# Kernel optimization log

Measured on AMD Instinct MI355X. Metric: run time of the kernel, lower is better.

Reference implementation:

```python
import jax, jax.numpy as jnp
import numpy as np

H_DIM = 768
NUM_HEADS = 12
HEAD_DIM = H_DIM // NUM_HEADS
ROPE_BASE = 10000.0


def rope_cos_sin(seq_len, dim):
    inv_freq = 1.0 / (ROPE_BASE ** (jnp.arange(0, dim, 2, dtype=jnp.float32) / dim))
    t = jnp.arange(seq_len, dtype=jnp.float32)
    freqs = jnp.outer(t, inv_freq)              # [seq, dim/2]
    emb = jnp.concatenate([freqs, freqs], axis=-1)  # [seq, dim]
    return jnp.cos(emb), jnp.sin(emb)


def rotate_half(x):
    x1, x2 = jnp.split(x, 2, axis=-1)
    return jnp.concatenate([-x2, x1], axis=-1)


def setup_inputs() -> dict:
    key = jax.random.key(0)
    ks = jax.random.split(key, 9)
    s = 1.0 / np.sqrt(H_DIM)
    inp = {
        'x': jax.random.normal(ks[0], (2, 8, 1024, H_DIM), dtype=jnp.float32),
        'Wq': jax.random.normal(ks[1], (H_DIM, H_DIM), dtype=jnp.float32) * s,
        'bq': jnp.zeros((H_DIM,), dtype=jnp.float32),
        'Wk': jax.random.normal(ks[2], (H_DIM, H_DIM), dtype=jnp.float32) * s,
        'bk': jnp.zeros((H_DIM,), dtype=jnp.float32),
        'Wv': jax.random.normal(ks[3], (H_DIM, H_DIM), dtype=jnp.float32) * s,
        'bv': jnp.zeros((H_DIM,), dtype=jnp.float32),
        'Wo': jax.random.normal(ks[4], (H_DIM, H_DIM), dtype=jnp.float32) * s,
        'bo': jnp.zeros((H_DIM,), dtype=jnp.float32),
        'mask': jnp.ones((2, 8, 1, 1, 1024), dtype=jnp.int32),
    }
    return inp


def reference(x, Wq, bq, Wk, bk, Wv, bv, Wo, bo, mask):
    b, r, s, d = x.shape
    H, D = NUM_HEADS, HEAD_DIM

    def proj(W, bvec):
        # [b,r,s,d] -> [b,r,H,s,D]
        y = x @ W + bvec
        return y.reshape(b, r, s, H, D).transpose(0, 1, 3, 2, 4)

    q = proj(Wq, bq)
    k = proj(Wk, bk)
    v = proj(Wv, bv)

    cos, sin = rope_cos_sin(s, D)   # [s, D]
    cos = cos[None, None, None]     # broadcast over b,r,H
    sin = sin[None, None, None]
    q = q * cos + rotate_half(q) * sin
    k = k * cos + rotate_half(k) * sin

    scores = jnp.einsum('brhqd,brhkd->brhqk', q, k) / jnp.sqrt(jnp.float32(D))
    scores = jnp.where(mask == 0, -jnp.inf, scores)
    probs = jax.nn.softmax(scores, axis=-1)  # dropout is identity in eval
    out = jnp.einsum('brhqk,brhkd->brhqd', probs, v)
    out = out.transpose(0, 1, 3, 2, 4).reshape(b, r, s, d)
    return out @ Wo + bo
```

## Files before the change

### kernel.cpp

```cpp
#include <hip/hip_runtime.h>


#define M_TOT 16384
#define DM    768
#define NH    12
#define HD    64
#define SEQ   1024

typedef __attribute__((ext_vector_type(8))) __bf16 bf16x8;
typedef __attribute__((ext_vector_type(4))) __bf16 bf16x4;
typedef __attribute__((ext_vector_type(4))) short s16x4;
typedef __attribute__((ext_vector_type(4))) float  f32x4;

static __device__ __forceinline__ unsigned short f2b(float f) {
  unsigned u = __builtin_bit_cast(unsigned, f);
  u += 0x7FFFu + ((u >> 16) & 1u);
  return (unsigned short)(u >> 16);
}
static __device__ __forceinline__ float b2f(unsigned short s) {
  unsigned u = ((unsigned)s) << 16;
  return __builtin_bit_cast(float, u);
}
static __device__ __forceinline__ unsigned cvt_pk_bf16(float lo, float hi) {
  unsigned d;
  asm("v_cvt_pk_bf16_f32 %0, %1, %2" : "=v"(d) : "v"(lo), "v"(hi));
  return d;
}
#define MAX3(a, b, c) fmaxf(fmaxf((a), (b)), (c))

static __device__ __forceinline__ f32x4 mfma16(uint2 a, uint2 b, f32x4 c) {
#if __has_builtin(__builtin_amdgcn_mfma_f32_16x16x16_bf16)
  union U { uint2 u; bf16x4 v; } A, B;
  A.u = a; B.u = b;
  return __builtin_amdgcn_mfma_f32_16x16x16_bf16(A.v, B.v, c, 0, 0, 0);
#else
  union U { uint2 u; s16x4 v; } A, B;
  A.u = a; B.u = b;
  return __builtin_amdgcn_mfma_f32_16x16x16bf16_1k(A.v, B.v, c, 0, 0, 0);
#endif
}

static __device__ __forceinline__ void gl_lds16(const void* g, void* l) {
  __builtin_amdgcn_global_load_lds(
      (const __attribute__((address_space(1))) unsigned*)g,
      (__attribute__((address_space(3))) unsigned*)l, 16, 0, 0);
}

static __device__ __forceinline__ int swz_src(int c) {
  return ((c >> 3) << 6) + (((c & 7) ^ ((c >> 3) & 7)) << 3);
}
static __device__ __forceinline__ int swz_rd(int row, int col16) {
  return (row << 6) + ((col16 ^ (row & 7)) << 3);
}

__global__ void cvt_x(const float* __restrict__ x, unsigned short* __restrict__ xb) {
  const int n4 = M_TOT * DM / 4;
  for (int i = blockIdx.x * blockDim.x + threadIdx.x; i < n4; i += gridDim.x * blockDim.x) {
    float4 v = ((const float4*)x)[i];
    ushort4 o;
    o.x = f2b(v.x); o.y = f2b(v.y); o.z = f2b(v.z); o.w = f2b(v.w);
    ((ushort4*)xb)[i] = o;
  }
}

__global__ void prep_w(const float* __restrict__ Wq, const float* __restrict__ Wk,
                       const float* __restrict__ Wv, const float* __restrict__ Wo,
                       unsigned short* __restrict__ Wt) {
  __shared__ float T[64][65];
  const int wsel = blockIdx.z;
  const float* W = wsel == 0 ? Wq : wsel == 1 ? Wk : wsel == 2 ? Wv : Wo;
  const int k0 = blockIdx.x * 64, n0 = blockIdx.y * 64;
  const int t = threadIdx.x;
#pragma unroll
  for (int p = 0; p < 16; ++p) {
    int e = p * 256 + t, r = e >> 6, c = e & 63;
    T[r][c] = W[(size_t)(k0 + r) * DM + n0 + c];
  }
  __syncthreads();
  unsigned short* dst = Wt + (size_t)wsel * DM * DM;
#pragma unroll
  for (int p = 0; p < 16; ++p) {
    int e = p * 256 + t, r = e >> 6, c = e & 63;
    dst[(size_t)(n0 + r) * DM + k0 + c] = f2b(T[c][r]);
  }
}

__global__ void rope_tab(float* __restrict__ cosT, float* __restrict__ sinT) {
  int i = blockIdx.x * blockDim.x + threadIdx.x;
  int s = i >> 5, j = i & 31;
  float inv = powf(10000.0f, -(float)j * (1.0f / 32.0f));
  float ang = (float)s * inv;
  cosT[i] = cosf(ang);
  sinT[i] = sinf(ang);
}

__global__ void bias_cat(const float* __restrict__ bq, const float* __restrict__ bk,
                         const float* __restrict__ bv, float* __restrict__ bcat) {
  int i = blockIdx.x * 256 + threadIdx.x;
  if (i < 3 * DM)
    bcat[i] = i < DM ? bq[i] : (i < 2 * DM ? bk[i - DM] : bv[i - 2 * DM]);
}

static __device__ __forceinline__ void gemm_core(const unsigned short* __restrict__ A,
                                                 const unsigned short* __restrict__ Bt,
                                                 int m0, int n0, f32x4 acc[4][4],
                                                 char* smem) {
  unsigned short* As = (unsigned short*)smem;
  unsigned short* Bs = As + 128 * 64;
  const int tid = threadIdx.x, lane = tid & 63, w = tid >> 6;
  const int wr = w >> 1, wc = w & 1;
  const int lr = lane & 15, g4 = lane >> 4;

#pragma unroll
  for (int i = 0; i < 4; ++i)
#pragma unroll
    for (int j = 0; j < 4; ++j) acc[i][j] = (f32x4){0.f, 0.f, 0.f, 0.f};

  for (int kt = 0; kt < DM / 64; ++kt) {
    const int k0 = kt * 64;
#pragma unroll
    for (int p = 0; p < 4; ++p) {
      int cb = p * 256 + w * 64;
      int c = cb + lane;
      gl_lds16(A + (size_t)(m0 + (c >> 3)) * DM + k0 + (c & 7) * 8, (char*)As + cb * 16);
      gl_lds16(Bt + (size_t)(n0 + (c >> 3)) * DM + k0 + (c & 7) * 8, (char*)Bs + cb * 16);
    }
    __syncthreads();
#pragma unroll
    for (int kk = 0; kk < 2; ++kk) {
      const int ko = kk * 32 + g4 * 8;
      bf16x8 a[4], b[4];
#pragma unroll
      for (int i = 0; i < 4; ++i) a[i] = *(const bf16x8*)&As[(wr * 64 + i * 16 + lr) * 64 + ko];
#pragma unroll
      for (int j = 0; j < 4; ++j) b[j] = *(const bf16x8*)&Bs[(wc * 64 + j * 16 + lr) * 64 + ko];
#pragma unroll
      for (int i = 0; i < 4; ++i)
#pragma unroll
        for (int j = 0; j < 4; ++j)
          acc[i][j] = __builtin_amdgcn_mfma_f32_16x16x32_bf16(a[i], b[j], acc[i][j], 0, 0, 0);
    }
    __syncthreads();
  }
}

__global__ __launch_bounds__(256, 4) void gemm_qkv(
    const unsigned short* __restrict__ xb, const unsigned short* __restrict__ Wt,
    const float* __restrict__ bcat, const float* __restrict__ cosT,
    const float* __restrict__ sinT, unsigned short* __restrict__ Qh,
    unsigned short* __restrict__ Kh, unsigned short* __restrict__ Vt) {
  __shared__ alignas(16) char smem[32768];
  const int id = blockIdx.x;
  const int xcdc = id & 7, rem = id >> 3;
  const int y = rem % 18, xc = rem / 18;
  const int xm = xc * 8 + xcdc;
  const int m0 = xm * 128, n0 = y * 128;
  f32x4 acc[4][4];
  gemm_core(xb, Wt, m0, n0, acc, smem);

  const int tid = threadIdx.x, lane = tid & 63, w = tid >> 6;
  const int wr = w >> 1, wc = w & 1;
  const int lr = lane & 15, g4 = lane >> 4;
  const int zone = y / 6;
  const int wcol0 = n0 - zone * DM + wc * 64;
  const int h = wcol0 >> 6;
  const int br = m0 >> 10;
  const int s_base = (m0 & 1023) + wr * 64;

  if (zone == 2) {
    unsigned short* dstb = Vt + ((size_t)(br * NH + h) * HD) * SEQ;
#pragma unroll
    for (int j = 0; j < 4; ++j) {
      const int d = j * 16 + lr;
      const float bv = bcat[n0 + wc * 64 + d];
#pragma unroll
      for (int i = 0; i < 4; ++i) {
        const int s0 = s_base + i * 16 + g4 * 4;
        ushort4 st;
        st.x = f2b(acc[i][j][0] + bv);
        st.y = f2b(acc[i][j][1] + bv);
        st.z = f2b(acc[i][j][2] + bv);
        st.w = f2b(acc[i][j][3] + bv);
        *(ushort4*)&dstb[(size_t)d * SEQ + s0] = st;
      }
    }
  } else {
    const float sc = zone == 0 ? 0.125f * 1.44269504f : 1.0f;
    unsigned short* dstb = (zone ? Kh : Qh) + ((size_t)(br * NH + h) * SEQ) * HD;
    char* Wb = smem + (size_t)w * 8192;
    const int s_q = s_base + lane;
    const int bcol = n0 + wc * 64;

#pragma unroll
    for (int hh = 0; hh < 2; ++hh) {
#pragma unroll
      for (int jj = 0; jj < 2; ++jj) {
        const int jp = hh + jj * 2;
        const float bv = bcat[bcol + jp * 16 + lr];
        const int dslot = jj * 16 + lr;
        const int sub = (dslot & 3) * 4;
        const int ch = dslot >> 2;
#pragma unroll
        for (int i = 0; i < 4; ++i) {
#pragma unroll
          for (int r = 0; r < 4; ++r) {
            const int s_loc = i * 16 + g4 * 4 + r;
            *(float*)(Wb + s_loc * 128 + ((ch ^ (s_loc & 7)) << 4) + sub) =
                (acc[i][jp][r] + bv) * sc;
          }
        }
      }
      unsigned short* drow = dstb + (size_t)s_q * HD + hh * 16;
      const char* Rb = Wb + lane * 128;
      const int lx = lane & 7;
#pragma unroll
      for (int c = 0; c < 4; ++c) {
        f32x4 va = *(const f32x4*)(Rb + ((c ^ lx) << 4));
        f32x4 vb = *(const f32x4*)(Rb + (((c + 4) ^ lx) << 4));
        float4 c4 = *(const float4*)&cosT[s_q * 32 + hh * 16 + c * 4];
        float4 s4 = *(const float4*)&sinT[s_q * 32 + hh * 16 + c * 4];
        uint2 oa, ob;
        oa.x = cvt_pk_bf16(va[0] * c4.x - vb[0] * s4.x, va[1] * c4.y - vb[1] * s4.y);
        oa.y = cvt_pk_bf16(va[2] * c4.z - vb[2] * s4.z, va[3] * c4.w - vb[3] * s4.w);
        ob.x = cvt_pk_bf16(vb[0] * c4.x + va[0] * s4.x, vb[1] * c4.y + va[1] * s4.y);
        ob.y = cvt_pk_bf16(vb[2] * c4.z + va[2] * s4.z, vb[3] * c4.w + va[3] * s4.w);
        *(uint2*)(drow + c * 4)      = oa;
        *(uint2*)(drow + 32 + c * 4) = ob;
      }
    }
  }
}

__global__ __launch_bounds__(256, 4) void gemm_o(const unsigned short* __restrict__ attnb,
                                                 const unsigned short* __restrict__ WtO,
                                                 const float* __restrict__ bo,
                                                 float* __restrict__ out) {
  __shared__ alignas(16) char smem[32768];
  const int id = blockIdx.x;
  const int xcdc = id & 7, rem = id >> 3;
  const int y = rem % 6, xc = rem / 6;
  const int m0 = (xc * 8 + xcdc) * 128, n0 = y * 128;
  f32x4 acc[4][4];
  gemm_core(attnb, WtO, m0, n0, acc, smem);
  const int tid = threadIdx.x, lane = tid & 63, w = tid >> 6;
  const int wr = w >> 1, wc = w & 1;
  const int lr = lane & 15, g4 = lane >> 4;
#pragma unroll
  for (int j = 0; j < 4; ++j) {
    const int col = n0 + wc * 64 + j * 16 + lr;
    const float bv = bo[col];
#pragma unroll
    for (int i = 0; i < 4; ++i) {
      const int rowb = m0 + wr * 64 + i * 16 + g4 * 4;
#pragma unroll
      for (int r = 0; r < 4; ++r)
        out[(size_t)(rowb + r) * DM + col] = acc[i][j][r] + bv;
    }
  }
}

__global__ __launch_bounds__(256) void attn_fwd(const unsigned short* __restrict__ Qh,
                                                const unsigned short* __restrict__ Kh,
                                                const unsigned short* __restrict__ Vt,
                                                const int* __restrict__ mask,
                                                unsigned short* __restrict__ attnb) {
  __shared__ unsigned short Ks[2][64 * 64];
  __shared__ unsigned short Vs[2][64 * 64];
  __shared__ float Msf[SEQ];
  const int id = blockIdx.x;
  const int xcdc = id & 7, rem = id >> 3;
  const int qt = rem & 15, g = rem >> 4;
  const int brh = g * 8 + xcdc;
  const int br = brh / NH, h = brh - br * NH;
  const int tid = threadIdx.x, lane = tid & 63, w = tid >> 6;
  const int lr = lane & 15, g4 = lane >> 4;

  const unsigned short* Kg = Kh + (size_t)brh * SEQ * HD;
  const unsigned short* Vg = Vt + (size_t)brh * HD * SEQ;

  int4 mi = *(const int4*)&mask[(size_t)br * SEQ + tid * 4];
  const int allLive = __syncthreads_and(mi.x && mi.y && mi.z && mi.w);
  if (!allLive) {
    float4 mf;
    mf.x = mi.x ? 0.f : -3e38f;
    mf.y = mi.y ? 0.f : -3e38f;
    mf.z = mi.z ? 0.f : -3e38f;
    mf.w = mi.w ? 0.f : -3e38f;
    *(float4*)&Msf[tid * 4] = mf;
  }

#pragma unroll
  for (int p = 0; p < 2; ++p) {
    int cb = p * 256 + w * 64;
    int c = cb + lane;
    gl_lds16(Kg + swz_src(c), (char*)Ks[0] + cb * 16);
    gl_lds16(Vg + (size_t)(c >> 3) * SEQ + (((c & 7) ^ ((c >> 3) & 7)) << 3),
             (char*)Vs[0] + cb * 16);
  }

  const unsigned short* Qg = Qh + ((size_t)brh * SEQ + qt * 64 + w * 16 + lr) * HD;
  bf16x8 qa[2];
  qa[0] = *(const bf16x8*)(Qg + g4 * 8);
  qa[1] = *(const bf16x8*)(Qg + 32 + g4 * 8);

  f32x4 o[4];
#pragma unroll
  for (int j = 0; j < 4; ++j) o[j] = (f32x4){0.f, 0.f, 0.f, 0.f};
  float m = -INFINITY;
  float lpA = 0.f, lpB = 0.f;

  __syncthreads();

  unsigned short* KsC = Ks[0];
  unsigned short* VsC = Vs[0];
  unsigned short* KsN = Ks[1];
  unsigned short* VsN = Vs[1];

  for (int kb = 0; kb < SEQ / 64; ++kb) {
    if (kb + 1 < SEQ / 64) {
#pragma unroll
      for (int p = 0; p < 2; ++p) {
        int cb = p * 256 + w * 64;
        int c = cb + lane;
        gl_lds16(Kg + (size_t)(kb + 1) * 64 * HD + swz_src(c), (char*)KsN + cb * 16);
        gl_lds16(Vg + (size_t)(c >> 3) * SEQ + (kb + 1) * 64 +
                     (((c & 7) ^ ((c >> 3) & 7)) << 3),
                 (char*)VsN + cb * 16);
      }
    }

    f32x4 s4[4];
#pragma unroll
    for (int j = 0; j < 4; ++j) s4[j] = (f32x4){0.f, 0.f, 0.f, 0.f};
    __builtin_amdgcn_s_setprio(1);
#pragma unroll
    for (int kk = 0; kk < 2; ++kk) {
#pragma unroll
      for (int j = 0; j < 4; ++j) {
        bf16x8 kf = *(const bf16x8*)&KsC[swz_rd(j * 16 + lr, kk * 4 + g4)];
        s4[j] = __builtin_amdgcn_mfma_f32_16x16x32_bf16(kf, qa[kk], s4[j], 0, 0, 0);
      }
    }
    __builtin_amdgcn_s_setprio(0);

    if (!allLive) {
#pragma unroll
      for (int j = 0; j < 4; ++j) {
        float4 mq = *(const float4*)&Msf[kb * 64 + j * 16 + g4 * 4];
        s4[j][0] += mq.x; s4[j][1] += mq.y; s4[j][2] += mq.z; s4[j][3] += mq.w;
      }
    }

    float t0 = MAX3(s4[0][0], s4[0][1], s4[0][2]);
    float t1 = MAX3(s4[0][3], s4[1][0], s4[1][1]);
    float t2 = MAX3(s4[1][2], s4[1][3], s4[2][0]);
    float t3 = MAX3(s4[2][1], s4[2][2], s4[2][3]);
    float t4 = MAX3(s4[3][0], s4[3][1], s4[3][2]);
    float mx = fmaxf(MAX3(t0, t1, s4[3][3]), MAX3(t2, t3, t4));
    mx = fmaxf(mx, __shfl_xor(mx, 16));
    mx = fmaxf(mx, __shfl_xor(mx, 32));
    if (!__all(mx <= m + 8.0f)) {
      float mnew = fmaxf(m, mx);
      float sc = exp2f(m - mnew);
      lpA *= sc; lpB *= sc;
#pragma unroll
      for (int j = 0; j < 4; ++j)
#pragma unroll
        for (int r = 0; r < 4; ++r) o[j][r] *= sc;
      m = mnew;
    }

    uint2 wb[4];
#pragma unroll
    for (int j = 0; j < 4; ++j) {
      float p0 = exp2f(s4[j][0] - m), p1 = exp2f(s4[j][1] - m);
      float p2 = exp2f(s4[j][2] - m), p3 = exp2f(s4[j][3] - m);
      if (j & 1) lpB += (p0 + p1) + (p2 + p3);
      else       lpA += (p0 + p1) + (p2 + p3);
      wb[j].x = cvt_pk_bf16(p0, p1);
      wb[j].y = cvt_pk_bf16(p2, p3);
    }

    __builtin_amdgcn_s_setprio(1);
#pragma unroll
    for (int jj = 0; jj < 4; ++jj) {
      const int row = jj * 16 + lr;
#pragma unroll
      for (int j = 0; j < 4; ++j) {
        const int c8 = j * 4 + g4;
        uint2 av = *(const uint2*)&VsC[(row << 6) + ((((c8 >> 1) ^ (lr & 7))) << 3) +
                                       ((c8 & 1) << 2)];
        o[jj] = mfma16(av, wb[j], o[jj]);
      }
    }
    __builtin_amdgcn_s_setprio(0);

    __syncthreads();
    unsigned short* t;
    t = KsC; KsC = KsN; KsN = t;
    t = VsC; VsC = VsN; VsN = t;
  }

  float lp = lpA + lpB;
  float l = lp + __shfl_xor(lp, 16);
  l += __shfl_xor(l, 32);
  float inv = l > 0.f ? 1.0f / l : 0.f;
  unsigned short* dst =
      attnb + ((size_t)(br * SEQ + qt * 64 + w * 16 + lr)) * DM + h * HD;
#pragma unroll
  for (int j = 0; j < 4; ++j) {
    ushort4 st;
    st.x = f2b(o[j][0] * inv);
    st.y = f2b(o[j][1] * inv);
    st.z = f2b(o[j][2] * inv);
    st.w = f2b(o[j][3] * inv);
    *(ushort4*)&dst[j * 16 + g4 * 4] = st;
  }
}

extern "C" void kernel_launch(void* const* d_in, const int* in_sizes, int n_in,
                              void* d_out, int out_size, void* d_ws, size_t ws_size,
                              hipStream_t stream) {
  const float* x  = (const float*)d_in[0];
  const float* Wq = (const float*)d_in[1];
  const float* bq = (const float*)d_in[2];
  const float* Wk = (const float*)d_in[3];
  const float* bk = (const float*)d_in[4];
  const float* Wv = (const float*)d_in[5];
  const float* bv = (const float*)d_in[6];
  const float* Wo = (const float*)d_in[7];
  const float* bo = (const float*)d_in[8];
  const int* mask = (const int*)d_in[9];
  float* out = (float*)d_out;

  const size_t OFF_XB   = 0;
  const size_t OFF_WT   = 25165824;
  const size_t OFF_COS  = 29884416;
  const size_t OFF_SIN  = 30015488;
  const size_t OFF_BC   = 30146560;
  const size_t OFF_ATT  = 30158848;
  const size_t OFF_QH   = 55324672;
  const size_t OFF_KH   = 80490496;
  const size_t OFF_VT   = 105656320;
  const size_t REQUIRED = 130822144;
  if (ws_size < REQUIRED) return;

  char* w = (char*)d_ws;
  unsigned short* xb   = (unsigned short*)(w + OFF_XB);
  unsigned short* Wt   = (unsigned short*)(w + OFF_WT);
  float* cosT          = (float*)(w + OFF_COS);
  float* sinT          = (float*)(w + OFF_SIN);
  float* bcat          = (float*)(w + OFF_BC);
  unsigned short* attnb = (unsigned short*)(w + OFF_ATT);
  unsigned short* Qh   = (unsigned short*)(w + OFF_QH);
  unsigned short* Kh   = (unsigned short*)(w + OFF_KH);
  unsigned short* Vt   = (unsigned short*)(w + OFF_VT);

  cvt_x<<<2048, 256, 0, stream>>>(x, xb);
  prep_w<<<dim3(12, 12, 4), 256, 0, stream>>>(Wq, Wk, Wv, Wo, Wt);
  rope_tab<<<128, 256, 0, stream>>>(cosT, sinT);
  bias_cat<<<9, 256, 0, stream>>>(bq, bk, bv, bcat);
  gemm_qkv<<<2304, 256, 0, stream>>>(xb, Wt, bcat, cosT, sinT, Qh, Kh, Vt);
  attn_fwd<<<3072, 256, 0, stream>>>(Qh, Kh, Vt, mask, attnb);
  gemm_o<<<768, 256, 0, stream>>>(attnb, Wt + (size_t)3 * DM * DM, bo, out);
}
```

Measured before the change: 264.8 us.

## Load K fragments directly into registers instead of staging through LDS

The attention kernel no longer stages K tiles in shared memory. Each lane loads its K MFMA fragments from global memory straight into registers, and prefetches the next tile after the QK MFMAs. The mask-bias LDS array is also dropped, with mask values read from global memory per block when masking is active. The launch bounds are set to target 5 blocks per CU. This frees LDS and removes LDS writes and reads for K, at the cost of more global and L2 traffic, since every wave reloads the same K tile. It also raises register pressure and exposes global-load latency to the next iteration.

```diff
diff --git a/kernel.cpp b/kernel.cpp
--- a/kernel.cpp
+++ b/kernel.cpp
@@ -48,9 +48,6 @@
 
 static __device__ __forceinline__ int swz_src(int c) {
   return ((c >> 3) << 6) + (((c & 7) ^ ((c >> 3) & 7)) << 3);
-}
-static __device__ __forceinline__ int swz_rd(int row, int col16) {
-  return (row << 6) + ((col16 ^ (row & 7)) << 3);
 }
 
 __global__ void cvt_x(const float* __restrict__ x, unsigned short* __restrict__ xb) {
@@ -259,14 +256,12 @@
   }
 }
 
-__global__ __launch_bounds__(256) void attn_fwd(const unsigned short* __restrict__ Qh,
-                                                const unsigned short* __restrict__ Kh,
-                                                const unsigned short* __restrict__ Vt,
-                                                const int* __restrict__ mask,
-                                                unsigned short* __restrict__ attnb) {
-  __shared__ unsigned short Ks[2][64 * 64];
+__global__ __launch_bounds__(256, 5) void attn_fwd(const unsigned short* __restrict__ Qh,
+                                                   const unsigned short* __restrict__ Kh,
+                                                   const unsigned short* __restrict__ Vt,
+                                                   const int* __restrict__ mask,
+                                                   unsigned short* __restrict__ attnb) {
   __shared__ unsigned short Vs[2][64 * 64];
-  __shared__ float Msf[SEQ];
   const int id = blockIdx.x;
   const int xcdc = id & 7, rem = id >> 3;
   const int qt = rem & 15, g = rem >> 4;
@@ -277,26 +272,26 @@
 
   const unsigned short* Kg = Kh + (size_t)brh * SEQ * HD;
   const unsigned short* Vg = Vt + (size_t)brh * HD * SEQ;
+  const int* mrow0 = mask + (size_t)br * SEQ + g4 * 4;
 
   int4 mi = *(const int4*)&mask[(size_t)br * SEQ + tid * 4];
   const int allLive = __syncthreads_and(mi.x && mi.y && mi.z && mi.w);
-  if (!allLive) {
-    float4 mf;
-    mf.x = mi.x ? 0.f : -3e38f;
-    mf.y = mi.y ? 0.f : -3e38f;
-    mf.z = mi.z ? 0.f : -3e38f;
-    mf.w = mi.w ? 0.f : -3e38f;
-    *(float4*)&Msf[tid * 4] = mf;
-  }
 
 #pragma unroll
   for (int p = 0; p < 2; ++p) {
     int cb = p * 256 + w * 64;
     int c = cb + lane;
-    gl_lds16(Kg + swz_src(c), (char*)Ks[0] + cb * 16);
     gl_lds16(Vg + (size_t)(c >> 3) * SEQ + (((c & 7) ^ ((c >> 3) & 7)) << 3),
              (char*)Vs[0] + cb * 16);
   }
+
+  const unsigned short* KgL = Kg + (size_t)lr * HD + g4 * 8;
+  bf16x8 kf[2][4];
+#pragma unroll
+  for (int kk = 0; kk < 2; ++kk)
+#pragma unroll
+    for (int j = 0; j < 4; ++j)
+      kf[kk][j] = *(const bf16x8*)(KgL + j * 16 * HD + kk * 32);
 
   const unsigned short* Qg = Qh + ((size_t)brh * SEQ + qt * 64 + w * 16 + lr) * HD;
   bf16x8 qa[2];
@@ -311,9 +306,7 @@
 
   __syncthreads();
 
-  unsigned short* KsC = Ks[0];
   unsigned short* VsC = Vs[0];
-  unsigned short* KsN = Ks[1];
   unsigned short* VsN = Vs[1];
 
   for (int kb = 0; kb < SEQ / 64; ++kb) {
@@ -322,7 +315,6 @@
       for (int p = 0; p < 2; ++p) {
         int cb = p * 256 + w * 64;
         int c = cb + lane;
-        gl_lds16(Kg + (size_t)(kb + 1) * 64 * HD + swz_src(c), (char*)KsN + cb * 16);
         gl_lds16(Vg + (size_t)(c >> 3) * SEQ + (kb + 1) * 64 +
                      (((c & 7) ^ ((c >> 3) & 7)) << 3),
                  (char*)VsN + cb * 16);
@@ -334,20 +326,30 @@
     for (int j = 0; j < 4; ++j) s4[j] = (f32x4){0.f, 0.f, 0.f, 0.f};
     __builtin_amdgcn_s_setprio(1);
 #pragma unroll
-    for (int kk = 0; kk < 2; ++kk) {
+    for (int kk = 0; kk < 2; ++kk)
+#pragma unroll
+      for (int j = 0; j < 4; ++j)
+        s4[j] = __builtin_amdgcn_mfma_f32_16x16x32_bf16(kf[kk][j], qa[kk], s4[j], 0, 0, 0);
+    __builtin_amdgcn_s_setprio(0);
+
+    if (kb + 1 < SEQ / 64) {
+      const unsigned short* Kn = KgL + (size_t)(kb + 1) * 64 * HD;
+#pragma unroll
+      for (int kk = 0; kk < 2; ++kk)
+#pragma unroll
+        for (int j = 0; j < 4; ++j)
+          kf[kk][j] = *(const bf16x8*)(Kn + j * 16 * HD + kk * 32);
+    }
+
+    if (!allLive) {
+      const int* mr = mrow0 + kb * 64;
 #pragma unroll
       for (int j = 0; j < 4; ++j) {
-        bf16x8 kf = *(const bf16x8*)&KsC[swz_rd(j * 16 + lr, kk * 4 + g4)];
-        s4[j] = __builtin_amdgcn_mfma_f32_16x16x32_bf16(kf, qa[kk], s4[j], 0, 0, 0);
-      }
-    }
-    __builtin_amdgcn_s_setprio(0);
-
-    if (!allLive) {
-#pragma unroll
-      for (int j = 0; j < 4; ++j) {
-        float4 mq = *(const float4*)&Msf[kb * 64 + j * 16 + g4 * 4];
-        s4[j][0] += mq.x; s4[j][1] += mq.y; s4[j][2] += mq.z; s4[j][3] += mq.w;
+        int4 mq = *(const int4*)&mr[j * 16];
+        s4[j][0] += mq.x ? 0.f : -3e38f;
+        s4[j][1] += mq.y ? 0.f : -3e38f;
+        s4[j][2] += mq.z ? 0.f : -3e38f;
+        s4[j][3] += mq.w ? 0.f : -3e38f;
       }
     }
 
@@ -397,7 +399,6 @@
 
     __syncthreads();
     unsigned short* t;
-    t = KsC; KsC = KsN; KsN = t;
     t = VsC; VsC = VsN; VsN = t;
   }
 
```

Measured after the change: 480.2 us. 1.81x slower.
